# Kernel optimization log

Measured on AMD Instinct MI355X. Metric: run time of the kernel, lower is better.

## Reference

```python
import jax, jax.numpy as jnp
import numpy as np


def setup_inputs() -> dict:
    key = jax.random.key(0)
    ks = jax.random.split(key, 8)
    B, H, W, C = 4, 64, 64, 64
    Cf = C // 8
    x = jax.random.normal(ks[0], (B, H, W, C), dtype=jnp.float32)
    # 1x1 conv kernels stored as [C_in, C_out] (kernel_size=1)
    w_f = jax.random.normal(ks[1], (C, Cf), dtype=jnp.float32) * 0.05
    b_f = jax.random.normal(ks[2], (Cf,), dtype=jnp.float32) * 0.05
    w_g = jax.random.normal(ks[3], (C, Cf), dtype=jnp.float32) * 0.05
    b_g = jax.random.normal(ks[4], (Cf,), dtype=jnp.float32) * 0.05
    w_h = jax.random.normal(ks[5], (C, C), dtype=jnp.float32) * 0.05
    b_h = jax.random.normal(ks[6], (C,), dtype=jnp.float32) * 0.05
    gamma = jax.random.normal(ks[7], (1,), dtype=jnp.float32) * 0.1
    return {"x": x, "w_f": w_f, "b_f": b_f, "w_g": w_g, "b_g": b_g,
            "w_h": w_h, "b_h": b_h, "gamma": gamma}


def reference(x, w_f, b_f, w_g, b_g, w_h, b_h, gamma):
    B, H, W, C = x.shape
    N = H * W
    xf = x.reshape(B, N, C)  # 1x1 conv == per-pixel linear
    f = xf @ w_f + b_f       # [B, N, C/8]
    g = xf @ w_g + b_g       # [B, N, C/8]
    h = xf @ w_h + b_h       # [B, N, C]
    # attention_map[b, i, j] = <g_i, f_j>, softmax over last axis
    scores = jnp.einsum('bic,bjc->bij', g, f)  # [B, N, N]
    attn = jax.nn.softmax(scores, axis=-1)
    out = jnp.einsum('bij,bjc->bic', attn, h)  # [B, N, C]
    out = out.reshape(B, H, W, C)
    return gamma * out + x
```

## Files before the change

kernel.cpp:

```cpp
#include <hip/hip_runtime.h>
#include <hip/hip_bf16.h>

typedef __bf16 bf16;
typedef __bf16 bf16x8 __attribute__((ext_vector_type(8)));
typedef __bf16 bf16x4 __attribute__((ext_vector_type(4)));
typedef float floatx4 __attribute__((ext_vector_type(4)));

typedef int  aint  __attribute__((may_alias));
typedef long along __attribute__((may_alias));

#define NPIX 4096
#define BATCH 4
#define LOG2E 1.4426950408889634f
#define HT_BATCH 262144

__device__ inline bf16x8 zero8() {
    bf16x8 v;
    #pragma unroll
    for (int i = 0; i < 8; ++i) v[i] = (bf16)0.0f;
    return v;
}

__global__ __launch_bounds__(256) void proj_kernel(
    const float* __restrict__ x,
    const float* __restrict__ w_f, const float* __restrict__ b_f,
    const float* __restrict__ w_g, const float* __restrict__ b_g,
    const float* __restrict__ w_h, const float* __restrict__ b_h,
    bf16* __restrict__ fq, bf16* __restrict__ gq, unsigned char* __restrict__ hT)
{
    __shared__ bf16 xs[64 * 72];
    __shared__ bf16 wt[80 * 72];
    __shared__ float bs[80];
    const int tid = threadIdx.x;
    const int p0 = blockIdx.x * 64;

    {
        const float4* xg = (const float4*)(x + (long)p0 * 64);
        #pragma unroll
        for (int it = 0; it < 4; ++it) {
            int i4 = tid + it * 256;
            float4 v = xg[i4];
            int row = i4 >> 4, c4 = (i4 & 15) * 4;
            bf16x4 pk;
            pk[0] = (bf16)v.x; pk[1] = (bf16)v.y; pk[2] = (bf16)v.z; pk[3] = (bf16)v.w;
            *(bf16x4*)(&xs[row * 72 + c4]) = pk;
        }
    }
    for (int idx = tid; idx < 512; idx += 256) {
        int c = idx >> 3, n = idx & 7;
        wt[n * 72 + c]       = (bf16)w_f[idx];
        wt[(8 + n) * 72 + c] = (bf16)w_g[idx];
    }
    #pragma unroll
    for (int it = 0; it < 16; ++it) {
        int idx = tid + it * 256;
        int c = idx >> 6, n = idx & 63;
        wt[(16 + n) * 72 + c] = (bf16)w_h[idx];
    }
    if (tid < 80)
        bs[tid] = (tid < 8) ? b_f[tid] : (tid < 16) ? b_g[tid - 8] : b_h[tid - 16];
    __syncthreads();

    const int wv = tid >> 6, lane = tid & 63;
    const int quad = lane >> 4, l15 = lane & 15;
    const int b = blockIdx.x >> 6;
    const int n0pix = (p0 & (NPIX - 1)) + wv * 16 + quad * 4;

    bf16x8 a0 = *(const bf16x8*)(&xs[(wv * 16 + l15) * 72 + quad * 8]);
    bf16x8 a1 = *(const bf16x8*)(&xs[(wv * 16 + l15) * 72 + 32 + quad * 8]);

    #pragma unroll
    for (int nt = 0; nt < 5; ++nt) {
        float bias = bs[nt * 16 + l15];
        floatx4 acc = {bias, bias, bias, bias};
        bf16x8 b0 = *(const bf16x8*)(&wt[(nt * 16 + l15) * 72 + quad * 8]);
        bf16x8 b1 = *(const bf16x8*)(&wt[(nt * 16 + l15) * 72 + 32 + quad * 8]);
        acc = __builtin_amdgcn_mfma_f32_16x16x32_bf16(a0, b0, acc, 0, 0, 0);
        acc = __builtin_amdgcn_mfma_f32_16x16x32_bf16(a1, b1, acc, 0, 0, 0);
        if (nt == 0) {
            #pragma unroll
            for (int r = 0; r < 4; ++r) {
                long P = (long)p0 + wv * 16 + quad * 4 + r;
                if (l15 < 8) fq[P * 8 + l15] = (bf16)acc[r];
                else         gq[P * 8 + (l15 - 8)] = (bf16)(acc[r] * LOG2E);
            }
        } else {
            int c = nt * 16 + l15 - 16;
            int pk = __builtin_amdgcn_cvt_pk_fp8_f32(acc[0], acc[1], 0, false);
            pk     = __builtin_amdgcn_cvt_pk_fp8_f32(acc[2], acc[3], pk, true);
            *(aint*)(hT + (long)b * HT_BATCH + (n0pix >> 5) * 2048
                     + c * 32 + (n0pix & 31)) = pk;
        }
    }
}

__global__ __launch_bounds__(512, 4) void attn_kernel(
    const bf16* __restrict__ fq, const bf16* __restrict__ gq,
    const unsigned char* __restrict__ hT, const float* __restrict__ x,
    const float* __restrict__ gamma_p, float* __restrict__ out)
{
    __shared__ float red[128 * 68];
    const int tid  = threadIdx.x;
    const int wv   = tid >> 6, lane = tid & 63;
    const int quad = lane >> 4, l15 = lane & 15;
    const int igrp = wv & 1, jq = wv >> 1;
    const int xcd = blockIdx.x & 7;
    const int b   = xcd >> 1;
    const int it  = ((blockIdx.x >> 3) & 63) | ((xcd & 1) << 6);
    const long rowbase = (long)b * NPIX + it * 32 + igrp * 16;
    const int jbase = jq * 1024;

    bf16x8 gfrag = zero8();
    if (lane < 16) gfrag = *(const bf16x8*)(gq + (rowbase + lane) * 8);

    const bf16* Fb = fq + ((long)b * NPIX + jbase) * 8;
    const unsigned char* Hb = hT + (long)b * HT_BATCH + (jbase >> 5) * 2048
                            + (l15 * 32 + quad * 8);

    floatx4 acc[5];
    #pragma unroll
    for (int nt = 0; nt < 5; ++nt) acc[nt] = (floatx4){0.f, 0.f, 0.f, 0.f};
    const along ones = 0x3838383838383838L;

    const int idx_lo = (((quad & 1) * 2) * 16 + l15) * 4;
    const int idx_hi = idx_lo + 64;
    const bool sel_b = (quad >> 1) != 0;

    for (int t = 0; t < 8; ++t) {
        bf16x8 af[8];
        #pragma unroll
        for (int j8 = 0; j8 < 8; ++j8) {
            af[j8] = zero8();
            if (lane < 16)
                af[j8] = *(const bf16x8*)(Fb + (t * 128 + j8 * 16 + l15) * 8);
        }
        along bfr[16];
        #pragma unroll
        for (int ks = 0; ks < 4; ++ks)
            #pragma unroll
            for (int nt = 0; nt < 4; ++nt)
                bfr[ks * 4 + nt] = *(const along*)(Hb + (t * 4 + ks) * 2048 + nt * 512);

        int pk[8];
        #pragma unroll
        for (int j8 = 0; j8 < 8; ++j8) {
            floatx4 s = __builtin_amdgcn_mfma_f32_16x16x32_bf16(
                af[j8], gfrag, (floatx4){0.f, 0.f, 0.f, 0.f}, 0, 0, 0);
            float e0 = __builtin_amdgcn_exp2f(s[0]);
            float e1 = __builtin_amdgcn_exp2f(s[1]);
            float e2 = __builtin_amdgcn_exp2f(s[2]);
            float e3 = __builtin_amdgcn_exp2f(s[3]);
            int p = __builtin_amdgcn_cvt_pk_fp8_f32(e0, e1, 0, false);
            pk[j8] = __builtin_amdgcn_cvt_pk_fp8_f32(e2, e3, p, true);
        }
        #pragma unroll
        for (int ks = 0; ks < 4; ++ks) {
            int pa = pk[2 * ks], pb = pk[2 * ks + 1];
            int lo0 = __builtin_amdgcn_ds_bpermute(idx_lo, pa);
            int lo1 = __builtin_amdgcn_ds_bpermute(idx_lo, pb);
            int hi0 = __builtin_amdgcn_ds_bpermute(idx_hi, pa);
            int hi1 = __builtin_amdgcn_ds_bpermute(idx_hi, pb);
            unsigned lo = (unsigned)(sel_b ? lo1 : lo0);
            unsigned hi = (unsigned)(sel_b ? hi1 : hi0);
            along pfrag = (along)(((unsigned long)hi << 32) | lo);
            #pragma unroll
            for (int nt = 0; nt < 4; ++nt)
                acc[nt] = __builtin_amdgcn_mfma_f32_16x16x32_fp8_fp8(
                    pfrag, bfr[ks * 4 + nt], acc[nt], 0, 0, 0);
            acc[4] = __builtin_amdgcn_mfma_f32_16x16x32_fp8_fp8(pfrag, ones, acc[4], 0, 0, 0);
        }
    }

    {
        const int rb = (jq * 32 + igrp * 16 + quad * 4) * 68;
        #pragma unroll
        for (int nt = 0; nt < 4; ++nt)
            #pragma unroll
            for (int r = 0; r < 4; ++r)
                red[rb + r * 68 + nt * 16 + l15] = acc[nt][r];
        if (l15 == 0) {
            #pragma unroll
            for (int r = 0; r < 4; ++r)
                red[rb + r * 68 + 64] = acc[4][r];
        }
    }
    __syncthreads();

    {
        const int row = tid >> 4, c0 = (tid & 15) * 4;
        float4 n = {0.f, 0.f, 0.f, 0.f};
        float den = 0.f;
        #pragma unroll
        for (int q = 0; q < 4; ++q) {
            const float* rr = red + (q * 32 + row) * 68;
            float4 v = *(const float4*)(rr + c0);
            n.x += v.x; n.y += v.y; n.z += v.z; n.w += v.w;
            den += rr[64];
        }
        const float rd = gamma_p[0] / den;
        const long off = ((long)b * NPIX + it * 32 + row) * 64 + c0;
        float4 xv = *(const float4*)(x + off);
        float4 o;
        o.x = n.x * rd + xv.x; o.y = n.y * rd + xv.y;
        o.z = n.z * rd + xv.z; o.w = n.w * rd + xv.w;
        *(float4*)(out + off) = o;
    }
}

extern "C" void kernel_launch(void* const* d_in, const int* in_sizes, int n_in,
                              void* d_out, int out_size, void* d_ws, size_t ws_size,
                              hipStream_t stream) {
    const float* x     = (const float*)d_in[0];
    const float* w_f   = (const float*)d_in[1];
    const float* b_f   = (const float*)d_in[2];
    const float* w_g   = (const float*)d_in[3];
    const float* b_g   = (const float*)d_in[4];
    const float* w_h   = (const float*)d_in[5];
    const float* b_h   = (const float*)d_in[6];
    const float* gamma = (const float*)d_in[7];
    float* out = (float*)d_out;

    bf16* fq = (bf16*)d_ws;
    bf16* gq = fq + 16384 * 8;
    unsigned char* hT = (unsigned char*)(gq + 16384 * 8);

    proj_kernel<<<256, 256, 0, stream>>>(x, w_f, b_f, w_g, b_g, w_h, b_h, fq, gq, hT);
    attn_kernel<<<512, 512, 0, stream>>>(fq, gq, hT, x, gamma, out);
}
```

Baseline: 97.00 us.

## Process two query row groups per wave and compute softmax denominator with VALU

Each wave now handles both 16-row query groups, so every F fragment and H tile it loads is reused for 32 rows. This halves global/L2 traffic for F and H and halves the block size to 256 threads. The softmax denominator is now summed in fp32 on the VALU and reduced with cross-lane shuffles, replacing the extra fp8 MFMA against an all-ones matrix. The cost is a higher register count per wave (8 accumulators, two sets of packed probabilities) and fewer waves per block to hide latency.

```diff
diff --git a/kernel.cpp b/kernel.cpp
--- a/kernel.cpp
+++ b/kernel.cpp
@@ -94,33 +94,36 @@
     }
 }
 
-__global__ __launch_bounds__(512, 4) void attn_kernel(
+__global__ __launch_bounds__(256, 4) void attn_kernel(
     const bf16* __restrict__ fq, const bf16* __restrict__ gq,
     const unsigned char* __restrict__ hT, const float* __restrict__ x,
     const float* __restrict__ gamma_p, float* __restrict__ out)
 {
-    __shared__ float red[128 * 68];
+    __shared__ float red[4 * 32 * 68];
     const int tid  = threadIdx.x;
     const int wv   = tid >> 6, lane = tid & 63;
     const int quad = lane >> 4, l15 = lane & 15;
-    const int igrp = wv & 1, jq = wv >> 1;
+    const int jq   = wv;
     const int xcd = blockIdx.x & 7;
     const int b   = xcd >> 1;
     const int it  = ((blockIdx.x >> 3) & 63) | ((xcd & 1) << 6);
-    const long rowbase = (long)b * NPIX + it * 32 + igrp * 16;
+    const long rowbase = (long)b * NPIX + it * 32;
     const int jbase = jq * 1024;
 
-    bf16x8 gfrag = zero8();
-    if (lane < 16) gfrag = *(const bf16x8*)(gq + (rowbase + lane) * 8);
+    bf16x8 gfragA = zero8(), gfragB = zero8();
+    if (lane < 16) {
+        gfragA = *(const bf16x8*)(gq + (rowbase + lane) * 8);
+        gfragB = *(const bf16x8*)(gq + (rowbase + 16 + lane) * 8);
+    }
 
     const bf16* Fb = fq + ((long)b * NPIX + jbase) * 8;
     const unsigned char* Hb = hT + (long)b * HT_BATCH + (jbase >> 5) * 2048
                             + (l15 * 32 + quad * 8);
 
-    floatx4 acc[5];
-    #pragma unroll
-    for (int nt = 0; nt < 5; ++nt) acc[nt] = (floatx4){0.f, 0.f, 0.f, 0.f};
-    const along ones = 0x3838383838383838L;
+    floatx4 acc[8];
+    #pragma unroll
+    for (int k = 0; k < 8; ++k) acc[k] = (floatx4){0.f, 0.f, 0.f, 0.f};
+    float denA = 0.f, denB = 0.f;
 
     const int idx_lo = (((quad & 1) * 2) * 16 + l15) * 4;
     const int idx_hi = idx_lo + 64;
@@ -141,69 +144,98 @@
             for (int nt = 0; nt < 4; ++nt)
                 bfr[ks * 4 + nt] = *(const along*)(Hb + (t * 4 + ks) * 2048 + nt * 512);
 
-        int pk[8];
+        int pkA[8], pkB[8];
         #pragma unroll
         for (int j8 = 0; j8 < 8; ++j8) {
-            floatx4 s = __builtin_amdgcn_mfma_f32_16x16x32_bf16(
-                af[j8], gfrag, (floatx4){0.f, 0.f, 0.f, 0.f}, 0, 0, 0);
-            float e0 = __builtin_amdgcn_exp2f(s[0]);
-            float e1 = __builtin_amdgcn_exp2f(s[1]);
-            float e2 = __builtin_amdgcn_exp2f(s[2]);
-            float e3 = __builtin_amdgcn_exp2f(s[3]);
-            int p = __builtin_amdgcn_cvt_pk_fp8_f32(e0, e1, 0, false);
-            pk[j8] = __builtin_amdgcn_cvt_pk_fp8_f32(e2, e3, p, true);
+            floatx4 sA = __builtin_amdgcn_mfma_f32_16x16x32_bf16(
+                af[j8], gfragA, (floatx4){0.f, 0.f, 0.f, 0.f}, 0, 0, 0);
+            floatx4 sB = __builtin_amdgcn_mfma_f32_16x16x32_bf16(
+                af[j8], gfragB, (floatx4){0.f, 0.f, 0.f, 0.f}, 0, 0, 0);
+            float a0 = __builtin_amdgcn_exp2f(sA[0]);
+            float a1 = __builtin_amdgcn_exp2f(sA[1]);
+            float a2 = __builtin_amdgcn_exp2f(sA[2]);
+            float a3 = __builtin_amdgcn_exp2f(sA[3]);
+            float b0 = __builtin_amdgcn_exp2f(sB[0]);
+            float b1 = __builtin_amdgcn_exp2f(sB[1]);
+            float b2 = __builtin_amdgcn_exp2f(sB[2]);
+            float b3 = __builtin_amdgcn_exp2f(sB[3]);
+            denA += (a0 + a1) + (a2 + a3);
+            denB += (b0 + b1) + (b2 + b3);
+            int pa = __builtin_amdgcn_cvt_pk_fp8_f32(a0, a1, 0, false);
+            pkA[j8] = __builtin_amdgcn_cvt_pk_fp8_f32(a2, a3, pa, true);
+            int pb = __builtin_amdgcn_cvt_pk_fp8_f32(b0, b1, 0, false);
+            pkB[j8] = __builtin_amdgcn_cvt_pk_fp8_f32(b2, b3, pb, true);
         }
         #pragma unroll
         for (int ks = 0; ks < 4; ++ks) {
-            int pa = pk[2 * ks], pb = pk[2 * ks + 1];
-            int lo0 = __builtin_amdgcn_ds_bpermute(idx_lo, pa);
-            int lo1 = __builtin_amdgcn_ds_bpermute(idx_lo, pb);
-            int hi0 = __builtin_amdgcn_ds_bpermute(idx_hi, pa);
-            int hi1 = __builtin_amdgcn_ds_bpermute(idx_hi, pb);
-            unsigned lo = (unsigned)(sel_b ? lo1 : lo0);
-            unsigned hi = (unsigned)(sel_b ? hi1 : hi0);
-            along pfrag = (along)(((unsigned long)hi << 32) | lo);
-            #pragma unroll
-            for (int nt = 0; nt < 4; ++nt)
-                acc[nt] = __builtin_amdgcn_mfma_f32_16x16x32_fp8_fp8(
-                    pfrag, bfr[ks * 4 + nt], acc[nt], 0, 0, 0);
-            acc[4] = __builtin_amdgcn_mfma_f32_16x16x32_fp8_fp8(pfrag, ones, acc[4], 0, 0, 0);
-        }
-    }
+            int loA0 = __builtin_amdgcn_ds_bpermute(idx_lo, pkA[2 * ks]);
+            int loA1 = __builtin_amdgcn_ds_bpermute(idx_lo, pkA[2 * ks + 1]);
+            int hiA0 = __builtin_amdgcn_ds_bpermute(idx_hi, pkA[2 * ks]);
+            int hiA1 = __builtin_amdgcn_ds_bpermute(idx_hi, pkA[2 * ks + 1]);
+            unsigned loA = (unsigned)(sel_b ? loA1 : loA0);
+            unsigned hiA = (unsigned)(sel_b ? hiA1 : hiA0);
+            along pfA = (along)(((unsigned long)hiA << 32) | loA);
+            int loB0 = __builtin_amdgcn_ds_bpermute(idx_lo, pkB[2 * ks]);
+            int loB1 = __builtin_amdgcn_ds_bpermute(idx_lo, pkB[2 * ks + 1]);
+            int hiB0 = __builtin_amdgcn_ds_bpermute(idx_hi, pkB[2 * ks]);
+            int hiB1 = __builtin_amdgcn_ds_bpermute(idx_hi, pkB[2 * ks + 1]);
+            unsigned loB = (unsigned)(sel_b ? loB1 : loB0);
+            unsigned hiB = (unsigned)(sel_b ? hiB1 : hiB0);
+            along pfB = (along)(((unsigned long)hiB << 32) | loB);
+            #pragma unroll
+            for (int nt = 0; nt < 4; ++nt) {
+                acc[nt]     = __builtin_amdgcn_mfma_f32_16x16x32_fp8_fp8(
+                    pfA, bfr[ks * 4 + nt], acc[nt], 0, 0, 0);
+                acc[4 + nt] = __builtin_amdgcn_mfma_f32_16x16x32_fp8_fp8(
+                    pfB, bfr[ks * 4 + nt], acc[4 + nt], 0, 0, 0);
+            }
+        }
+    }
+
+    denA += __shfl_xor(denA, 16);  denA += __shfl_xor(denA, 32);
+    denB += __shfl_xor(denB, 16);  denB += __shfl_xor(denB, 32);
 
     {
-        const int rb = (jq * 32 + igrp * 16 + quad * 4) * 68;
+        const int rbA = (jq * 32 + quad * 4) * 68;
+        const int rbB = (jq * 32 + 16 + quad * 4) * 68;
         #pragma unroll
         for (int nt = 0; nt < 4; ++nt)
             #pragma unroll
-            for (int r = 0; r < 4; ++r)
-                red[rb + r * 68 + nt * 16 + l15] = acc[nt][r];
-        if (l15 == 0) {
-            #pragma unroll
-            for (int r = 0; r < 4; ++r)
-                red[rb + r * 68 + 64] = acc[4][r];
+            for (int r = 0; r < 4; ++r) {
+                red[rbA + r * 68 + nt * 16 + l15] = acc[nt][r];
+                red[rbB + r * 68 + nt * 16 + l15] = acc[4 + nt][r];
+            }
+        if (quad == 0) {
+            red[(jq * 32 + l15) * 68 + 64]      = denA;
+            red[(jq * 32 + 16 + l15) * 68 + 64] = denB;
         }
     }
     __syncthreads();
 
     {
-        const int row = tid >> 4, c0 = (tid & 15) * 4;
-        float4 n = {0.f, 0.f, 0.f, 0.f};
+        const int row = tid >> 3, c0 = (tid & 7) * 8;
+        float4 n0 = {0.f, 0.f, 0.f, 0.f}, n1 = {0.f, 0.f, 0.f, 0.f};
         float den = 0.f;
         #pragma unroll
         for (int q = 0; q < 4; ++q) {
             const float* rr = red + (q * 32 + row) * 68;
-            float4 v = *(const float4*)(rr + c0);
-            n.x += v.x; n.y += v.y; n.z += v.z; n.w += v.w;
+            float4 a = *(const float4*)(rr + c0);
+            float4 c = *(const float4*)(rr + c0 + 4);
+            n0.x += a.x; n0.y += a.y; n0.z += a.z; n0.w += a.w;
+            n1.x += c.x; n1.y += c.y; n1.z += c.z; n1.w += c.w;
             den += rr[64];
         }
         const float rd = gamma_p[0] / den;
-        const long off = ((long)b * NPIX + it * 32 + row) * 64 + c0;
-        float4 xv = *(const float4*)(x + off);
-        float4 o;
-        o.x = n.x * rd + xv.x; o.y = n.y * rd + xv.y;
-        o.z = n.z * rd + xv.z; o.w = n.w * rd + xv.w;
-        *(float4*)(out + off) = o;
+        const long off = (rowbase + row) * 64 + c0;
+        float4 xa = *(const float4*)(x + off);
+        float4 xb = *(const float4*)(x + off + 4);
+        float4 oa, ob;
+        oa.x = n0.x * rd + xa.x; oa.y = n0.y * rd + xa.y;
+        oa.z = n0.z * rd + xa.z; oa.w = n0.w * rd + xa.w;
+        ob.x = n1.x * rd + xb.x; ob.y = n1.y * rd + xb.y;
+        ob.z = n1.z * rd + xb.z; ob.w = n1.w * rd + xb.w;
+        *(float4*)(out + off) = oa;
+        *(float4*)(out + off + 4) = ob;
     }
 }
 
@@ -225,5 +257,5 @@
     unsigned char* hT = (unsigned char*)(gq + 16384 * 8);
 
     proj_kernel<<<256, 256, 0, stream>>>(x, w_f, b_f, w_g, b_g, w_h, b_h, fq, gq, hT);
-    attn_kernel<<<512, 512, 0, stream>>>(fq, gq, hT, x, gamma, out);
-}
+    attn_kernel<<<512, 256, 0, stream>>>(fq, gq, hT, x, gamma, out);
+}
```

New measurement: 95.57 us. About the same (-1.5%).
